# Kernel tuning notes

Measured on AMD Instinct MI355X. Metric: run time of the kernel, lower is better.

## Reference

```python
import jax, jax.numpy as jnp
import numpy as np

HIDDEN = 2048
N_HEADS = 16
HEAD_DIM = HIDDEN // N_HEADS
INV_NORM = 1.0 / float(np.sqrt(HEAD_DIM))
BETA = 1.0


def setup_inputs() -> dict:
    key = jax.random.key(0)
    ks = jax.random.split(key, 12)
    B, S, H = 2, 2048, HIDDEN
    scale = 1.0 / float(np.sqrt(H))
    return {
        "hidden_states": jax.random.normal(ks[0], (B, S, H), jnp.float32),
        "residual": jax.random.normal(ks[1], (B, S, H), jnp.float32),
        "alibi": jax.random.normal(ks[2], (B * N_HEADS, 1, S), jnp.float32),
        "Wq": jax.random.normal(ks[3], (H, H), jnp.float32) * scale,
        "bq": jnp.zeros((H,), jnp.float32),
        "Wk": jax.random.normal(ks[4], (H, H), jnp.float32) * scale,
        "bk": jnp.zeros((H,), jnp.float32),
        "Wv": jax.random.normal(ks[5], (H, H), jnp.float32) * scale,
        "bv": jnp.zeros((H,), jnp.float32),
        "Wd": jax.random.normal(ks[6], (H, H), jnp.float32) * scale,
        "bd": jnp.zeros((H,), jnp.float32),
    }


def reference(hidden_states, residual, alibi, Wq, bq, Wk, bk, Wv, bv, Wd, bd):
    B, S, H = hidden_states.shape
    # separate QKV projections (nn.Linear: x @ W^T + b)
    q = hidden_states @ Wq.T + bq
    k = hidden_states @ Wk.T + bk
    v = hidden_states @ Wv.T + bv
    # [B, n_heads, S, head_dim]
    q = q.reshape(B, S, N_HEADS, HEAD_DIM).transpose(0, 2, 1, 3)
    k = k.reshape(B, S, N_HEADS, HEAD_DIM).transpose(0, 2, 1, 3)
    v = v.reshape(B, S, N_HEADS, HEAD_DIM).transpose(0, 2, 1, 3)
    # baddbmm: scores = beta * alibi + inv_norm * q @ k^T, per (batch*head)
    alibi_bh = alibi.reshape(B, N_HEADS, 1, S)  # broadcasts over query dim
    scores = BETA * alibi_bh + INV_NORM * jnp.einsum("bhqd,bhkd->bhqk", q, k)
    probs = jax.nn.softmax(scores.astype(jnp.float32), axis=-1).astype(v.dtype)
    # attention dropout: p=0.0 (identity)
    ctx = jnp.einsum("bhqk,bhkd->bhqd", probs, v)  # [B,H,S,D]
    ctx = ctx.transpose(0, 2, 1, 3).reshape(B, S, H)
    out = ctx @ Wd.T + bd
    # hidden dropout p=0.0 then residual add (dropout_add)
    return out + residual
```

## Files before the change

### kernel.cpp

```cpp
#include <hip/hip_runtime.h>

#define HID   2048
#define NHEAD 16
#define HD    128
#define SEQ   2048
#define BATCH 2
#define MROWS (BATCH*SEQ)
#define NQKV  (3*HID)
#define INV_NORM 0.08838834764831845f
#define LOG2E    1.4426950408889634f
#define SCALE_L2 (INV_NORM*LOG2E)

typedef __attribute__((ext_vector_type(8)))  __bf16 bf16x8;
typedef __attribute__((ext_vector_type(4)))  float  f32x4;
typedef __attribute__((ext_vector_type(16))) float  f32x16;

typedef __attribute__((address_space(1))) void GV;
typedef __attribute__((address_space(3))) void LV;

__device__ __forceinline__ void async16(const void* g, void* l) {
  __builtin_amdgcn_global_load_lds((const GV*)g, (LV*)l, 16, 0, 0);
}

__device__ __forceinline__ unsigned short f2bf(float f) {
  unsigned u = __builtin_bit_cast(unsigned, f);
  u += 0x7FFFu + ((u >> 16) & 1u);
  return (unsigned short)(u >> 16);
}

__device__ __forceinline__ unsigned pkbf(float a, float b) {
#if __has_builtin(__builtin_amdgcn_cvt_pk_bf16_f32)
  typedef __attribute__((ext_vector_type(2))) __bf16 bf16x2;
  bf16x2 r = __builtin_amdgcn_cvt_pk_bf16_f32(a, b);
  return __builtin_bit_cast(unsigned, r);
#else
  return (unsigned)f2bf(a) | ((unsigned)f2bf(b) << 16);
#endif
}

__device__ __forceinline__ void mfma16(f32x4& c, bf16x8 a, bf16x8 b) {
  c = __builtin_amdgcn_mfma_f32_16x16x32_bf16(a, b, c, 0, 0, 0);
}

__device__ __forceinline__ bf16x8 frag(const unsigned short* buf, int row, int chunk) {
  return *(const bf16x8*)(buf + ((row * 8 + (chunk ^ (row & 7))) << 3));
}

__global__ __launch_bounds__(256) void cvt_kernel(const float* __restrict__ src,
                                                  unsigned short* __restrict__ dst, int n) {
  int i = (blockIdx.x * 256 + threadIdx.x) * 4;
  if (i >= n) return;
  float4 v = *(const float4*)(src + i);
  ushort4 o;
  o.x = f2bf(v.x); o.y = f2bf(v.y); o.z = f2bf(v.z); o.w = f2bf(v.w);
  *(ushort4*)(dst + i) = o;
}

__global__ __launch_bounds__(256) void cvtw_kernel(const float* __restrict__ W0,
                                                   const float* __restrict__ W1,
                                                   const float* __restrict__ W2,
                                                   const float* __restrict__ W3,
                                                   unsigned short* __restrict__ dst) {
  int sel = blockIdx.y;
  const float* src = (sel == 0) ? W0 : (sel == 1) ? W1 : (sel == 2) ? W2 : W3;
  unsigned short* d = dst + (size_t)sel * HID * HID;
  int i = (blockIdx.x * 256 + threadIdx.x) * 4;
  float4 v = *(const float4*)(src + i);
  ushort4 o;
  o.x = f2bf(v.x); o.y = f2bf(v.y); o.z = f2bf(v.z); o.w = f2bf(v.w);
  *(ushort4*)(d + i) = o;
}

__device__ __forceinline__ void gemm_core(const unsigned short* __restrict__ A,
                                          const unsigned short* __restrict__ Bm,
                                          int K, int m0, int n0,
                                          unsigned short* As, unsigned short* Bs,
                                          f32x4 (&acc)[4][4]) {
  const int tid  = threadIdx.x;
  const int w    = tid >> 6;
  const int lane = tid & 63;
  const int l16  = lane & 15;
  const int quad = lane >> 4;
  const int wm   = (w & 1) * 64;
  const int wn   = (w >> 1) * 64;

  const f32x4 zero = {0.f, 0.f, 0.f, 0.f};
#pragma unroll
  for (int i = 0; i < 4; ++i)
#pragma unroll
    for (int j = 0; j < 4; ++j) acc[i][j] = zero;

  for (int k0 = 0; k0 < K; k0 += 64) {
    __syncthreads();
#pragma unroll
    for (int i = 0; i < 4; ++i) {
      int slot = i * 256 + w * 64 + lane;
      int r = slot >> 3;
      int c = (slot & 7) ^ (r & 7);
      async16(A  + (size_t)(m0 + r) * K + k0 + c * 8, (char*)As + (size_t)(i * 256 + w * 64) * 16);
      async16(Bm + (size_t)(n0 + r) * K + k0 + c * 8, (char*)Bs + (size_t)(i * 256 + w * 64) * 16);
    }
    __syncthreads();

#pragma unroll
    for (int kk = 0; kk < 2; ++kk) {
      bf16x8 af[4], bfp[4];
#pragma unroll
      for (int i = 0; i < 4; ++i) af[i]  = frag(As, wm + i * 16 + l16, kk * 4 + quad);
#pragma unroll
      for (int j = 0; j < 4; ++j) bfp[j] = frag(Bs, wn + j * 16 + l16, kk * 4 + quad);
#pragma unroll
      for (int i = 0; i < 4; ++i)
#pragma unroll
        for (int j = 0; j < 4; ++j) mfma16(acc[i][j], af[i], bfp[j]);
    }
  }
}

#define BUFU (24576)
#define BUF3 (3 * BUFU)

__global__ __launch_bounds__(512, 2) void gemm_qkv384_kernel(
    const unsigned short* __restrict__ Xb, const unsigned short* __restrict__ Wb,
    const float* __restrict__ bq, const float* __restrict__ bk,
    const float* __restrict__ bv, unsigned short* __restrict__ Cout) {
  __shared__ __align__(16) unsigned short smem[BUF3];

  const int tid  = threadIdx.x;
  const int w    = tid >> 6;
  const int lane = tid & 63;
  const int l16  = lane & 15;
  const int quad = lane >> 4;
  const int wm   = (w & 3) * 64;
  const int wn   = (w >> 2) * 64;

  const int wg = blockIdx.x;
  const int sw = (wg & 7) * 32 + (wg >> 3);
  const int m0  = (sw & 15) * 256;
  const int rn0 = (sw >> 4) * 384;

  const int sr  = tid >> 3;
  const int scs = ((tid & 7) ^ (sr & 7)) * 8;
  const unsigned short* aBase = Xb + (size_t)(m0 + sr) * HID + scs;

#define STGA(UB, RB, KT)                                              \
  async16(aBase + (size_t)(RB) * HID + (KT),                          \
          (char*)smem + (UB) * 2 + (RB) * 128 + w * 1024)
#define STGB(UB, RB, KT)                                              \
  async16(bBase + (size_t)(RB) * HID + (KT),                          \
          (char*)smem + (UB) * 2 + 32768 + (RB) * 128 + w * 1024)

#define VM6  asm volatile("s_waitcnt vmcnt(6)" ::: "memory")
#define VM0  asm volatile("s_waitcnt vmcnt(0)" ::: "memory")

#define PHASE(UB, KK, STGBLK, WAITBLK)                                         \
  {                                                                            \
    const unsigned short* Ab = smem + (UB);                                    \
    const unsigned short* Bb = Ab + 16384;                                     \
    bf16x8 ta[4], tb[4];                                                       \
    ta[0] = frag(Ab, wm + l16, (KK) * 4 + quad);                               \
    _Pragma("unroll")                                                          \
    for (int j = 0; j < 4; ++j)  tb[j] = frag(Bb, wn + j * 16 + l16, (KK) * 4 + quad); \
    _Pragma("unroll")                                                          \
    for (int ii = 1; ii < 4; ++ii) ta[ii] = frag(Ab, wm + ii * 16 + l16, (KK) * 4 + quad); \
    STGBLK;                                                                    \
    __builtin_amdgcn_s_setprio(1);                                             \
    _Pragma("unroll")                                                          \
    for (int ii = 0; ii < 4; ++ii)                                             \
      _Pragma("unroll")                                                        \
      for (int j = 0; j < 4; ++j) mfma16(acc[ii][j], ta[ii], tb[j]);           \
    __builtin_amdgcn_s_setprio(0);                                             \
    asm volatile("s_waitcnt lgkmcnt(0)" ::: "memory");                         \
    WAITBLK;                                                                   \
    __builtin_amdgcn_s_barrier();                                              \
  }

  for (int p = 0; p < 3; ++p) {
    const unsigned short* bBase = Wb + (size_t)(rn0 + p * 128 + sr) * HID + scs;

    f32x4 acc[4][4];
    const f32x4 zero = {0.f, 0.f, 0.f, 0.f};
#pragma unroll
    for (int a = 0; a < 4; ++a)
#pragma unroll
      for (int j = 0; j < 4; ++j) acc[a][j] = zero;

    STGA(0, 0, 0);  STGA(0, 64, 0);  STGA(0, 128, 0);  STGA(0, 192, 0);
    STGB(0, 0, 0);  STGB(0, 64, 0);
    STGA(BUFU, 0, 64);  STGA(BUFU, 64, 64);  STGA(BUFU, 128, 64);  STGA(BUFU, 192, 64);
    STGB(BUFU, 0, 64);  STGB(BUFU, 64, 64);
    VM6;
    __builtin_amdgcn_s_barrier();

    int kb = 0;
    for (int g = 0; g < 5; ++g) {
      PHASE(0,        0, { STGA(2*BUFU, 0, kb+128); STGA(2*BUFU, 64, kb+128); STGA(2*BUFU, 128, kb+128); }, {});
      PHASE(0,        1, { STGA(2*BUFU, 192, kb+128); STGB(2*BUFU, 0, kb+128); STGB(2*BUFU, 64, kb+128); }, VM6);
      PHASE(BUFU,     0, { STGA(0, 0, kb+192); STGA(0, 64, kb+192); STGA(0, 128, kb+192); }, {});
      PHASE(BUFU,     1, { STGA(0, 192, kb+192); STGB(0, 0, kb+192); STGB(0, 64, kb+192); }, VM6);
      PHASE(2*BUFU,   0, { STGA(BUFU, 0, kb+256); STGA(BUFU, 64, kb+256); STGA(BUFU, 128, kb+256); }, {});
      PHASE(2*BUFU,   1, { STGA(BUFU, 192, kb+256); STGB(BUFU, 0, kb+256); STGB(BUFU, 64, kb+256); }, VM6);
      PHASE(0,        0, { STGA(2*BUFU, 0, kb+320); STGA(2*BUFU, 64, kb+320); STGA(2*BUFU, 128, kb+320); }, {});
      PHASE(0,        1, { STGA(2*BUFU, 192, kb+320); STGB(2*BUFU, 0, kb+320); STGB(2*BUFU, 64, kb+320); }, VM6);
      PHASE(BUFU,     0, { STGA(0, 0, kb+384); STGA(0, 64, kb+384); STGA(0, 128, kb+384); }, {});
      PHASE(BUFU,     1, { STGA(0, 192, kb+384); STGB(0, 0, kb+384); STGB(0, 64, kb+384); }, VM6);
      PHASE(2*BUFU,   0, { STGA(BUFU, 0, kb+448); STGA(BUFU, 64, kb+448); STGA(BUFU, 128, kb+448); }, {});
      PHASE(2*BUFU,   1, { STGA(BUFU, 192, kb+448); STGB(BUFU, 0, kb+448); STGB(BUFU, 64, kb+448); }, VM6);
      kb += 384;
    }

    PHASE(0,    0, {}, {});
    PHASE(0,    1, {}, VM0);
    PHASE(BUFU, 0, {}, {});
    PHASE(BUFU, 1, {}, {});

#pragma unroll
    for (int j = 0; j < 4; ++j) {
      int ng = rn0 + p * 128 + wn + j * 16 + l16;
      float bias = (ng < HID) ? bq[ng] : (ng < 2 * HID ? bk[ng - HID] : bv[ng - 2 * HID]);
#pragma unroll
      for (int a = 0; a < 4; ++a)
#pragma unroll
        for (int r = 0; r < 4; ++r) {
          int mg = m0 + wm + a * 16 + quad * 4 + r;
          Cout[(size_t)mg * NQKV + ng] = f2bf(acc[a][j][r] + bias);
        }
    }
  }
#undef STGA
#undef STGB
#undef PHASE
#undef VM6
#undef VM0
}

__global__ __launch_bounds__(256) void gemm_out_kernel(
    const unsigned short* __restrict__ Ctx, const unsigned short* __restrict__ Wdb,
    const float* __restrict__ bd, const float* __restrict__ Res,
    float* __restrict__ Out) {
  __shared__ __align__(16) unsigned short As[128 * 64];
  __shared__ __align__(16) unsigned short Bs[128 * 64];
  f32x4 acc[4][4];
  const int m0 = blockIdx.y * 128, n0 = blockIdx.x * 128;
  gemm_core(Ctx, Wdb, HID, m0, n0, As, Bs, acc);

  const int tid = threadIdx.x, w = tid >> 6, lane = tid & 63;
  const int l16 = lane & 15, quad = lane >> 4;
  const int wm = (w & 1) * 64, wn = (w >> 1) * 64;
#pragma unroll
  for (int j = 0; j < 4; ++j) {
    int ng = n0 + wn + j * 16 + l16;
    float bias = bd[ng];
#pragma unroll
    for (int i = 0; i < 4; ++i)
#pragma unroll
      for (int r = 0; r < 4; ++r) {
        int mg = m0 + wm + i * 16 + quad * 4 + r;
        size_t off = (size_t)mg * HID + ng;
        Out[off] = acc[i][j][r] + bias + Res[off];
      }
  }
}

__global__ __launch_bounds__(256) void vtrans_kernel(const unsigned short* __restrict__ QKV,
                                                     unsigned short* __restrict__ Vt) {
  __shared__ __align__(16) unsigned short T[64][72];
  const int s0 = blockIdx.x * 64, d0 = blockIdx.y * 64, bh = blockIdx.z;
  const int b = bh >> 4, h = bh & 15;
  const int tid = threadIdx.x;
#pragma unroll
  for (int i = 0; i < 2; ++i) {
    int idx = i * 256 + tid;
    int r = idx >> 3, ch = idx & 7;
    const unsigned short* g = QKV + ((size_t)b * SEQ + s0 + r) * NQKV + 2 * HID + h * HD + d0 + ch * 8;
    *(uint4*)(&T[r][ch * 8]) = *(const uint4*)g;
  }
  __syncthreads();
#pragma unroll
  for (int i = 0; i < 2; ++i) {
    int idx = i * 256 + tid;
    int d = idx >> 3, ch = idx & 7;
    unsigned short v[8];
#pragma unroll
    for (int x = 0; x < 8; ++x) v[x] = T[ch * 8 + x][d];
    unsigned short* g = Vt + ((size_t)bh * HD + d0 + d) * SEQ + s0 + ch * 8;
    *(uint4*)g = *(const uint4*)v;
  }
}

__global__ __launch_bounds__(256, 2) void attn_kernel(
    const unsigned short* __restrict__ QKV, const unsigned short* __restrict__ Vt,
    const float* __restrict__ alibi, unsigned short* __restrict__ Ctx) {
  __shared__ __align__(16) char smem[51200];
  unsigned short* Ks  = (unsigned short*)smem;
  unsigned short* Vts = (unsigned short*)(smem + 16384);
  unsigned short* Ps  = (unsigned short*)(smem + 32768);
  unsigned short* Qs  = (unsigned short*)smem;

  const int tid = threadIdx.x, w = tid >> 6, lane = tid & 63;
  const int l32 = lane & 31, h = lane >> 5;
  const int q0 = blockIdx.x * 128;
  const int bh = blockIdx.y, b = bh >> 4, hh = bh & 15;
  const size_t rowbase = (size_t)b * SEQ;
  const float* ali = alibi + (size_t)bh * SEQ;
  const unsigned short* Vbh = Vt + (size_t)bh * HD * SEQ;

  {
    const unsigned short* qbase = QKV + (rowbase + q0) * NQKV + hh * HD;
#pragma unroll
    for (int i = 0; i < 8; ++i) {
      int slot = i * 256 + w * 64 + lane;
      int r = slot >> 4, c = (slot & 15) ^ (r & 15);
      async16(qbase + (size_t)r * NQKV + c * 8, (char*)Qs + (size_t)(i * 256 + w * 64) * 16);
    }
  }
  __syncthreads();
  bf16x8 qf[8];
  {
    int qr = w * 32 + l32;
#pragma unroll
    for (int ks = 0; ks < 8; ++ks) {
      int c = (ks * 2 + h) ^ (qr & 15);
      qf[ks] = *(const bf16x8*)(Qs + (qr * 16 + c) * 8);
    }
  }

  f32x16 oacc[4];
  float l_acc = 0.f;
#pragma unroll
  for (int nb = 0; nb < 4; ++nb)
#pragma unroll
    for (int r = 0; r < 16; ++r) oacc[nb][r] = 0.f;

  __syncthreads();

  for (int kt = 0; kt < SEQ / 64; ++kt) {
    {
      const unsigned short* kbase = QKV + (rowbase + kt * 64) * NQKV + HID + hh * HD;
#pragma unroll
      for (int i = 0; i < 4; ++i) {
        int slot = i * 256 + w * 64 + lane;
        int r = slot >> 4, c = (slot & 15) ^ (r & 15);
        async16(kbase + (size_t)r * NQKV + c * 8, (char*)Ks + (size_t)(i * 256 + w * 64) * 16);
      }
      const unsigned short* vbase = Vbh + kt * 64;
#pragma unroll
      for (int i = 0; i < 4; ++i) {
        int slot = i * 256 + w * 64 + lane;
        int r = slot >> 3, c = (slot & 7) ^ (r & 7);
        async16(vbase + (size_t)r * SEQ + c * 8, (char*)Vts + (size_t)(i * 256 + w * 64) * 16);
      }
    }
    __syncthreads();

    f32x16 sacc[2];
#pragma unroll
    for (int mb = 0; mb < 2; ++mb)
#pragma unroll
      for (int r = 0; r < 16; ++r) sacc[mb][r] = 0.f;
#pragma unroll
    for (int ks = 0; ks < 8; ++ks) {
#pragma unroll
      for (int mb = 0; mb < 2; ++mb) {
        bf16x8 kf = *(const bf16x8*)(Ks + ((mb * 32 + l32) * 16 + ((ks * 2 + h) ^ (l32 & 15))) * 8);
        sacc[mb] = __builtin_amdgcn_mfma_f32_32x32x16_bf16(kf, qf[ks], sacc[mb], 0, 0, 0);
      }
    }

    const float* alik = ali + kt * 64 + 4 * h;
    const int qrow = w * 32 + l32;
#pragma unroll
    for (int mb = 0; mb < 2; ++mb) {
#pragma unroll
      for (int g = 0; g < 4; ++g) {
        float4 av = *(const float4*)(alik + mb * 32 + g * 8);
        float p0 = __builtin_amdgcn_exp2f(sacc[mb][g * 4 + 0] * SCALE_L2 + av.x * LOG2E);
        float p1 = __builtin_amdgcn_exp2f(sacc[mb][g * 4 + 1] * SCALE_L2 + av.y * LOG2E);
        float p2 = __builtin_amdgcn_exp2f(sacc[mb][g * 4 + 2] * SCALE_L2 + av.z * LOG2E);
        float p3 = __builtin_amdgcn_exp2f(sacc[mb][g * 4 + 3] * SCALE_L2 + av.w * LOG2E);
        l_acc += (p0 + p1) + (p2 + p3);
        uint2 pk;
        pk.x = pkbf(p0, p1);
        pk.y = pkbf(p2, p3);
        *(uint2*)(Ps + qrow * 72 + mb * 32 + g * 8 + 4 * h) = pk;
      }
    }

#pragma unroll
    for (int ks2 = 0; ks2 < 4; ++ks2) {
      bf16x8 pf = *(const bf16x8*)(Ps + qrow * 72 + ks2 * 16 + h * 8);
#pragma unroll
      for (int nb = 0; nb < 4; ++nb) {
        bf16x8 vf = *(const bf16x8*)(Vts + ((nb * 32 + l32) * 8 + ((ks2 * 2 + h) ^ (l32 & 7))) * 8);
        oacc[nb] = __builtin_amdgcn_mfma_f32_32x32x16_bf16(pf, vf, oacc[nb], 0, 0, 0);
      }
    }
    __syncthreads();
  }

  float lf = l_acc + __shfl_xor(l_acc, 32, 64);
  float rinv[16];
#pragma unroll
  for (int reg = 0; reg < 16; ++reg) {
    int row = (reg & 3) + 8 * (reg >> 2) + 4 * h;
    rinv[reg] = 1.0f / __shfl(lf, row, 64);
  }

#pragma unroll
  for (int nb = 0; nb < 4; ++nb)
#pragma unroll
    for (int reg = 0; reg < 16; ++reg) {
      int row = (reg & 3) + 8 * (reg >> 2) + 4 * h;
      size_t qg = rowbase + q0 + w * 32 + row;
      Ctx[qg * HID + hh * HD + nb * 32 + l32] = f2bf(oacc[nb][reg] * rinv[reg]);
    }
}

extern "C" void kernel_launch(void* const* d_in, const int* in_sizes, int n_in,
                              void* d_out, int out_size, void* d_ws, size_t ws_size,
                              hipStream_t stream) {
  const float* hidden   = (const float*)d_in[0];
  const float* residual = (const float*)d_in[1];
  const float* alibi    = (const float*)d_in[2];
  const float* Wq = (const float*)d_in[3];
  const float* bq = (const float*)d_in[4];
  const float* Wk = (const float*)d_in[5];
  const float* bk = (const float*)d_in[6];
  const float* Wv = (const float*)d_in[7];
  const float* bv = (const float*)d_in[8];
  const float* Wd = (const float*)d_in[9];
  const float* bd = (const float*)d_in[10];
  float* out = (float*)d_out;

  unsigned short* Xb    = (unsigned short*)d_ws;
  unsigned short* Wqkvb = Xb + (size_t)MROWS * HID;
  unsigned short* Wdb   = Wqkvb + (size_t)NQKV * HID;
  unsigned short* QKVb  = Wdb + (size_t)HID * HID;
  unsigned short* Ctxb  = QKVb + (size_t)MROWS * NQKV;
  unsigned short* Vtb   = Wqkvb;

  const int nX = MROWS * HID, nW = HID * HID;
  cvt_kernel<<<nX / 4 / 256, 256, 0, stream>>>(hidden, Xb, nX);
  cvtw_kernel<<<dim3(nW / 4 / 256, 4), 256, 0, stream>>>(Wq, Wk, Wv, Wd, Wqkvb);

  gemm_qkv384_kernel<<<256, 512, 0, stream>>>(Xb, Wqkvb, bq, bk, bv, QKVb);
  vtrans_kernel<<<dim3(SEQ / 64, HD / 64, BATCH * NHEAD), 256, 0, stream>>>(QKVb, Vtb);
  attn_kernel<<<dim3(SEQ / 128, BATCH * NHEAD), 256, 0, stream>>>(QKVb, Vtb, alibi, Ctxb);
  gemm_out_kernel<<<dim3(HID / 128, MROWS / 128), 256, 0, stream>>>(Ctxb, Wdb, bd, residual, out);
}
```

Measured before the change: 437.4 us.

## Pipeline out-projection GEMM with triple buffering and prefetch K/V in attention

Replaces the simple synchronous out-projection GEMM with a 512-thread, 256x128-tile kernel that uses a triple-buffered async LDS pipeline, a swizzled block order and MFMA priority hints, modelled on the QKV GEMM. In the attention kernel, the next K tile and a double-buffered V tile are prefetched while the current tile's softmax and PV work runs, and alibi is staged in LDS once. These changes aim to hide global-memory latency behind compute. The cost is higher LDS use (about 74 KB per attention block), which may lower occupancy.

```diff
diff --git a/kernel.cpp b/kernel.cpp
--- a/kernel.cpp
+++ b/kernel.cpp
@@ -69,52 +69,6 @@
   ushort4 o;
   o.x = f2bf(v.x); o.y = f2bf(v.y); o.z = f2bf(v.z); o.w = f2bf(v.w);
   *(ushort4*)(d + i) = o;
-}
-
-__device__ __forceinline__ void gemm_core(const unsigned short* __restrict__ A,
-                                          const unsigned short* __restrict__ Bm,
-                                          int K, int m0, int n0,
-                                          unsigned short* As, unsigned short* Bs,
-                                          f32x4 (&acc)[4][4]) {
-  const int tid  = threadIdx.x;
-  const int w    = tid >> 6;
-  const int lane = tid & 63;
-  const int l16  = lane & 15;
-  const int quad = lane >> 4;
-  const int wm   = (w & 1) * 64;
-  const int wn   = (w >> 1) * 64;
-
-  const f32x4 zero = {0.f, 0.f, 0.f, 0.f};
-#pragma unroll
-  for (int i = 0; i < 4; ++i)
-#pragma unroll
-    for (int j = 0; j < 4; ++j) acc[i][j] = zero;
-
-  for (int k0 = 0; k0 < K; k0 += 64) {
-    __syncthreads();
-#pragma unroll
-    for (int i = 0; i < 4; ++i) {
-      int slot = i * 256 + w * 64 + lane;
-      int r = slot >> 3;
-      int c = (slot & 7) ^ (r & 7);
-      async16(A  + (size_t)(m0 + r) * K + k0 + c * 8, (char*)As + (size_t)(i * 256 + w * 64) * 16);
-      async16(Bm + (size_t)(n0 + r) * K + k0 + c * 8, (char*)Bs + (size_t)(i * 256 + w * 64) * 16);
-    }
-    __syncthreads();
-
-#pragma unroll
-    for (int kk = 0; kk < 2; ++kk) {
-      bf16x8 af[4], bfp[4];
-#pragma unroll
-      for (int i = 0; i < 4; ++i) af[i]  = frag(As, wm + i * 16 + l16, kk * 4 + quad);
-#pragma unroll
-      for (int j = 0; j < 4; ++j) bfp[j] = frag(Bs, wn + j * 16 + l16, kk * 4 + quad);
-#pragma unroll
-      for (int i = 0; i < 4; ++i)
-#pragma unroll
-        for (int j = 0; j < 4; ++j) mfma16(acc[i][j], af[i], bfp[j]);
-    }
-  }
 }
 
 #define BUFU (24576)
@@ -234,32 +188,116 @@
 #undef VM0
 }
 
-__global__ __launch_bounds__(256) void gemm_out_kernel(
+__global__ __launch_bounds__(512, 2) void gemm_out384_kernel(
     const unsigned short* __restrict__ Ctx, const unsigned short* __restrict__ Wdb,
     const float* __restrict__ bd, const float* __restrict__ Res,
     float* __restrict__ Out) {
-  __shared__ __align__(16) unsigned short As[128 * 64];
-  __shared__ __align__(16) unsigned short Bs[128 * 64];
+  __shared__ __align__(16) unsigned short smem[BUF3];
+
+  const int tid  = threadIdx.x;
+  const int w    = tid >> 6;
+  const int lane = tid & 63;
+  const int l16  = lane & 15;
+  const int quad = lane >> 4;
+  const int wm   = (w & 3) * 64;
+  const int wn   = (w >> 2) * 64;
+
+  const int wg = blockIdx.x;
+  const int sw = (wg & 7) * 32 + (wg >> 3);
+  const int m0  = (sw & 15) * 256;
+  const int rn0 = (sw >> 4) * 128;
+
+  const int sr  = tid >> 3;
+  const int scs = ((tid & 7) ^ (sr & 7)) * 8;
+  const unsigned short* aBase = Ctx + (size_t)(m0 + sr) * HID + scs;
+  const unsigned short* bBase = Wdb + (size_t)(rn0 + sr) * HID + scs;
+
+#define STGA(UB, RB, KT)                                              \
+  async16(aBase + (size_t)(RB) * HID + (KT),                          \
+          (char*)smem + (UB) * 2 + (RB) * 128 + w * 1024)
+#define STGB(UB, RB, KT)                                              \
+  async16(bBase + (size_t)(RB) * HID + (KT),                          \
+          (char*)smem + (UB) * 2 + 32768 + (RB) * 128 + w * 1024)
+
+#define VM6  asm volatile("s_waitcnt vmcnt(6)" ::: "memory")
+#define VM0  asm volatile("s_waitcnt vmcnt(0)" ::: "memory")
+
+#define PHASE(UB, KK, STGBLK, WAITBLK)                                         \
+  {                                                                            \
+    const unsigned short* Ab = smem + (UB);                                    \
+    const unsigned short* Bb = Ab + 16384;                                     \
+    bf16x8 ta[4], tb[4];                                                       \
+    ta[0] = frag(Ab, wm + l16, (KK) * 4 + quad);                               \
+    _Pragma("unroll")                                                          \
+    for (int j = 0; j < 4; ++j)  tb[j] = frag(Bb, wn + j * 16 + l16, (KK) * 4 + quad); \
+    _Pragma("unroll")                                                          \
+    for (int ii = 1; ii < 4; ++ii) ta[ii] = frag(Ab, wm + ii * 16 + l16, (KK) * 4 + quad); \
+    STGBLK;                                                                    \
+    __builtin_amdgcn_s_setprio(1);                                             \
+    _Pragma("unroll")                                                          \
+    for (int ii = 0; ii < 4; ++ii)                                             \
+      _Pragma("unroll")                                                        \
+      for (int j = 0; j < 4; ++j) mfma16(acc[ii][j], ta[ii], tb[j]);           \
+    __builtin_amdgcn_s_setprio(0);                                             \
+    asm volatile("s_waitcnt lgkmcnt(0)" ::: "memory");                         \
+    WAITBLK;                                                                   \
+    __builtin_amdgcn_s_barrier();                                              \
+  }
+
   f32x4 acc[4][4];
-  const int m0 = blockIdx.y * 128, n0 = blockIdx.x * 128;
-  gemm_core(Ctx, Wdb, HID, m0, n0, As, Bs, acc);
-
-  const int tid = threadIdx.x, w = tid >> 6, lane = tid & 63;
-  const int l16 = lane & 15, quad = lane >> 4;
-  const int wm = (w & 1) * 64, wn = (w >> 1) * 64;
+  const f32x4 zero = {0.f, 0.f, 0.f, 0.f};
+#pragma unroll
+  for (int a = 0; a < 4; ++a)
+#pragma unroll
+    for (int j = 0; j < 4; ++j) acc[a][j] = zero;
+
+  STGA(0, 0, 0);  STGA(0, 64, 0);  STGA(0, 128, 0);  STGA(0, 192, 0);
+  STGB(0, 0, 0);  STGB(0, 64, 0);
+  STGA(BUFU, 0, 64);  STGA(BUFU, 64, 64);  STGA(BUFU, 128, 64);  STGA(BUFU, 192, 64);
+  STGB(BUFU, 0, 64);  STGB(BUFU, 64, 64);
+  VM6;
+  __builtin_amdgcn_s_barrier();
+
+  int kb = 0;
+  for (int g = 0; g < 5; ++g) {
+    PHASE(0,        0, { STGA(2*BUFU, 0, kb+128); STGA(2*BUFU, 64, kb+128); STGA(2*BUFU, 128, kb+128); }, {});
+    PHASE(0,        1, { STGA(2*BUFU, 192, kb+128); STGB(2*BUFU, 0, kb+128); STGB(2*BUFU, 64, kb+128); }, VM6);
+    PHASE(BUFU,     0, { STGA(0, 0, kb+192); STGA(0, 64, kb+192); STGA(0, 128, kb+192); }, {});
+    PHASE(BUFU,     1, { STGA(0, 192, kb+192); STGB(0, 0, kb+192); STGB(0, 64, kb+192); }, VM6);
+    PHASE(2*BUFU,   0, { STGA(BUFU, 0, kb+256); STGA(BUFU, 64, kb+256); STGA(BUFU, 128, kb+256); }, {});
+    PHASE(2*BUFU,   1, { STGA(BUFU, 192, kb+256); STGB(BUFU, 0, kb+256); STGB(BUFU, 64, kb+256); }, VM6);
+    PHASE(0,        0, { STGA(2*BUFU, 0, kb+320); STGA(2*BUFU, 64, kb+320); STGA(2*BUFU, 128, kb+320); }, {});
+    PHASE(0,        1, { STGA(2*BUFU, 192, kb+320); STGB(2*BUFU, 0, kb+320); STGB(2*BUFU, 64, kb+320); }, VM6);
+    PHASE(BUFU,     0, { STGA(0, 0, kb+384); STGA(0, 64, kb+384); STGA(0, 128, kb+384); }, {});
+    PHASE(BUFU,     1, { STGA(0, 192, kb+384); STGB(0, 0, kb+384); STGB(0, 64, kb+384); }, VM6);
+    PHASE(2*BUFU,   0, { STGA(BUFU, 0, kb+448); STGA(BUFU, 64, kb+448); STGA(BUFU, 128, kb+448); }, {});
+    PHASE(2*BUFU,   1, { STGA(BUFU, 192, kb+448); STGB(BUFU, 0, kb+448); STGB(BUFU, 64, kb+448); }, VM6);
+    kb += 384;
+  }
+
+  PHASE(0,    0, {}, {});
+  PHASE(0,    1, {}, VM0);
+  PHASE(BUFU, 0, {}, {});
+  PHASE(BUFU, 1, {}, {});
+
 #pragma unroll
   for (int j = 0; j < 4; ++j) {
-    int ng = n0 + wn + j * 16 + l16;
+    int ng = rn0 + wn + j * 16 + l16;
     float bias = bd[ng];
 #pragma unroll
-    for (int i = 0; i < 4; ++i)
+    for (int a = 0; a < 4; ++a)
 #pragma unroll
       for (int r = 0; r < 4; ++r) {
-        int mg = m0 + wm + i * 16 + quad * 4 + r;
+        int mg = m0 + wm + a * 16 + quad * 4 + r;
         size_t off = (size_t)mg * HID + ng;
-        Out[off] = acc[i][j][r] + bias + Res[off];
+        Out[off] = acc[a][j][r] + bias + Res[off];
       }
   }
+#undef STGA
+#undef STGB
+#undef PHASE
+#undef VM6
+#undef VM0
 }
 
 __global__ __launch_bounds__(256) void vtrans_kernel(const unsigned short* __restrict__ QKV,
@@ -291,11 +329,13 @@
 __global__ __launch_bounds__(256, 2) void attn_kernel(
     const unsigned short* __restrict__ QKV, const unsigned short* __restrict__ Vt,
     const float* __restrict__ alibi, unsigned short* __restrict__ Ctx) {
-  __shared__ __align__(16) char smem[51200];
-  unsigned short* Ks  = (unsigned short*)smem;
-  unsigned short* Vts = (unsigned short*)(smem + 16384);
-  unsigned short* Ps  = (unsigned short*)(smem + 32768);
-  unsigned short* Qs  = (unsigned short*)smem;
+  __shared__ __align__(16) char smem[75776];
+  unsigned short* Ks   = (unsigned short*)smem;
+  unsigned short* Vts0 = (unsigned short*)(smem + 16384);
+  unsigned short* Vts1 = (unsigned short*)(smem + 32768);
+  unsigned short* Ps   = (unsigned short*)(smem + 49152);
+  float*          Alsf = (float*)(smem + 67584);
+  unsigned short* Qs   = (unsigned short*)smem;
 
   const int tid = threadIdx.x, w = tid >> 6, lane = tid & 63;
   const int l32 = lane & 31, h = lane >> 5;
@@ -313,6 +353,12 @@
       int r = slot >> 4, c = (slot & 15) ^ (r & 15);
       async16(qbase + (size_t)r * NQKV + c * 8, (char*)Qs + (size_t)(i * 256 + w * 64) * 16);
     }
+    const char* asrc = (const char*)ali;
+#pragma unroll
+    for (int i = 0; i < 2; ++i) {
+      int slot = i * 256 + w * 64 + lane;
+      async16(asrc + (size_t)slot * 16, (char*)Alsf + (size_t)(i * 256 + w * 64) * 16);
+    }
   }
   __syncthreads();
   bf16x8 qf[8];
@@ -334,46 +380,67 @@
 
   __syncthreads();
 
+  {
+    const unsigned short* kbase = QKV + rowbase * NQKV + HID + hh * HD;
+#pragma unroll
+    for (int i = 0; i < 4; ++i) {
+      int slot = i * 256 + w * 64 + lane;
+      int r = slot >> 4, c = (slot & 15) ^ (r & 15);
+      async16(kbase + (size_t)r * NQKV + c * 8, (char*)Ks + (size_t)(i * 256 + w * 64) * 16);
+    }
+#pragma unroll
+    for (int i = 0; i < 4; ++i) {
+      int slot = i * 256 + w * 64 + lane;
+      int r = slot >> 3, c = (slot & 7) ^ (r & 7);
+      async16(Vbh + (size_t)r * SEQ + c * 8, (char*)Vts0 + (size_t)(i * 256 + w * 64) * 16);
+    }
+  }
+  __syncthreads();
+
   for (int kt = 0; kt < SEQ / 64; ++kt) {
-    {
-      const unsigned short* kbase = QKV + (rowbase + kt * 64) * NQKV + HID + hh * HD;
+    f32x16 sacc[2];
+#pragma unroll
+    for (int mb = 0; mb < 2; ++mb)
+#pragma unroll
+      for (int r = 0; r < 16; ++r) sacc[mb][r] = 0.f;
+    __builtin_amdgcn_s_setprio(1);
+#pragma unroll
+    for (int ks = 0; ks < 8; ++ks) {
+#pragma unroll
+      for (int mb = 0; mb < 2; ++mb) {
+        bf16x8 kf = *(const bf16x8*)(Ks + ((mb * 32 + l32) * 16 + ((ks * 2 + h) ^ (l32 & 15))) * 8);
+        sacc[mb] = __builtin_amdgcn_mfma_f32_32x32x16_bf16(kf, qf[ks], sacc[mb], 0, 0, 0);
+      }
+    }
+    __builtin_amdgcn_s_setprio(0);
+    asm volatile("s_waitcnt lgkmcnt(0)" ::: "memory");
+    __builtin_amdgcn_s_barrier();
+
+    if (kt + 1 < SEQ / 64) {
+      const unsigned short* kbase = QKV + (rowbase + (kt + 1) * 64) * NQKV + HID + hh * HD;
 #pragma unroll
       for (int i = 0; i < 4; ++i) {
         int slot = i * 256 + w * 64 + lane;
         int r = slot >> 4, c = (slot & 15) ^ (r & 15);
         async16(kbase + (size_t)r * NQKV + c * 8, (char*)Ks + (size_t)(i * 256 + w * 64) * 16);
       }
-      const unsigned short* vbase = Vbh + kt * 64;
+      const unsigned short* vbase = Vbh + (kt + 1) * 64;
+      unsigned short* vdst = ((kt + 1) & 1) ? Vts1 : Vts0;
 #pragma unroll
       for (int i = 0; i < 4; ++i) {
         int slot = i * 256 + w * 64 + lane;
         int r = slot >> 3, c = (slot & 7) ^ (r & 7);
-        async16(vbase + (size_t)r * SEQ + c * 8, (char*)Vts + (size_t)(i * 256 + w * 64) * 16);
+        async16(vbase + (size_t)r * SEQ + c * 8, (char*)vdst + (size_t)(i * 256 + w * 64) * 16);
       }
     }
-    __syncthreads();
-
-    f32x16 sacc[2];
-#pragma unroll
-    for (int mb = 0; mb < 2; ++mb)
-#pragma unroll
-      for (int r = 0; r < 16; ++r) sacc[mb][r] = 0.f;
-#pragma unroll
-    for (int ks = 0; ks < 8; ++ks) {
-#pragma unroll
-      for (int mb = 0; mb < 2; ++mb) {
-        bf16x8 kf = *(const bf16x8*)(Ks + ((mb * 32 + l32) * 16 + ((ks * 2 + h) ^ (l32 & 15))) * 8);
-        sacc[mb] = __builtin_amdgcn_mfma_f32_32x32x16_bf16(kf, qf[ks], sacc[mb], 0, 0, 0);
-      }
-    }
-
-    const float* alik = ali + kt * 64 + 4 * h;
+
     const int qrow = w * 32 + l32;
+    const float* alsk = Alsf + kt * 64 + 4 * h;
 #pragma unroll
     for (int mb = 0; mb < 2; ++mb) {
 #pragma unroll
       for (int g = 0; g < 4; ++g) {
-        float4 av = *(const float4*)(alik + mb * 32 + g * 8);
+        float4 av = *(const float4*)(alsk + mb * 32 + g * 8);
         float p0 = __builtin_amdgcn_exp2f(sacc[mb][g * 4 + 0] * SCALE_L2 + av.x * LOG2E);
         float p1 = __builtin_amdgcn_exp2f(sacc[mb][g * 4 + 1] * SCALE_L2 + av.y * LOG2E);
         float p2 = __builtin_amdgcn_exp2f(sacc[mb][g * 4 + 2] * SCALE_L2 + av.z * LOG2E);
@@ -386,16 +453,21 @@
       }
     }
 
+    const unsigned short* vcur = (kt & 1) ? Vts1 : Vts0;
+    __builtin_amdgcn_s_setprio(1);
 #pragma unroll
     for (int ks2 = 0; ks2 < 4; ++ks2) {
       bf16x8 pf = *(const bf16x8*)(Ps + qrow * 72 + ks2 * 16 + h * 8);
 #pragma unroll
       for (int nb = 0; nb < 4; ++nb) {
-        bf16x8 vf = *(const bf16x8*)(Vts + ((nb * 32 + l32) * 8 + ((ks2 * 2 + h) ^ (l32 & 7))) * 8);
+        bf16x8 vf = *(const bf16x8*)(vcur + ((nb * 32 + l32) * 8 + ((ks2 * 2 + h) ^ (l32 & 7))) * 8);
         oacc[nb] = __builtin_amdgcn_mfma_f32_32x32x16_bf16(pf, vf, oacc[nb], 0, 0, 0);
       }
     }
-    __syncthreads();
+    __builtin_amdgcn_s_setprio(0);
+
+    asm volatile("s_waitcnt lgkmcnt(0) vmcnt(0)" ::: "memory");
+    __builtin_amdgcn_s_barrier();
   }
 
   float lf = l_acc + __shfl_xor(l_acc, 32, 64);
@@ -446,5 +518,5 @@
   gemm_qkv384_kernel<<<256, 512, 0, stream>>>(Xb, Wqkvb, bq, bk, bv, QKVb);
   vtrans_kernel<<<dim3(SEQ / 64, HD / 64, BATCH * NHEAD), 256, 0, stream>>>(QKVb, Vtb);
   attn_kernel<<<dim3(SEQ / 128, BATCH * NHEAD), 256, 0, stream>>>(QKVb, Vtb, alibi, Ctxb);
-  gemm_out_kernel<<<dim3(HID / 128, MROWS / 128), 256, 0, stream>>>(Ctxb, Wdb, bd, residual, out);
-}
+  gemm_out384_kernel<<<256, 512, 0, stream>>>(Ctxb, Wdb, bd, residual, out);
+}
```

Result: no change. 444.1 us (+1.5%).
